# Performance work log

Hardware: AMD Instinct MI355X
Metric: run time of the kernel (lower is better)

## Reference

```python
import jax, jax.numpy as jnp
import numpy as np

N, E, D_IN, D_H, D_OUT = 100000, 1600000, 128, 128, 47
BN_EPS = 1e-5


def setup_inputs() -> dict:
    key = jax.random.key(0)
    ks = jax.random.split(key, 12)
    x = jax.random.normal(ks[0], (N, D_IN), dtype=jnp.float32)
    edge_index = jax.random.randint(ks[1], (2, E), 0, N, dtype=jnp.int64)
    s = 1.0 / np.sqrt(D_H)
    return {
        "x": x,
        "edge_index": edge_index,
        "W1": jax.random.normal(ks[2], (D_IN, D_H), dtype=jnp.float32) * s,
        "b1": jnp.zeros((D_H,), dtype=jnp.float32),
        "gamma": jax.random.uniform(ks[3], (D_H,), dtype=jnp.float32, minval=0.5, maxval=1.5),
        "beta": jax.random.normal(ks[4], (D_H,), dtype=jnp.float32) * 0.1,
        "mean": jax.random.normal(ks[5], (D_H,), dtype=jnp.float32) * 0.1,
        "var": jax.random.uniform(ks[6], (D_H,), dtype=jnp.float32, minval=0.5, maxval=1.5),
        "W2": jax.random.normal(ks[7], (D_H, D_H), dtype=jnp.float32) * s,
        "b2": jnp.zeros((D_H,), dtype=jnp.float32),
        "Wf": jax.random.normal(ks[8], (D_H, D_OUT), dtype=jnp.float32) * s,
        "bf": jnp.zeros((D_OUT,), dtype=jnp.float32),
    }


def gcn_conv(x, src, dst, W, b, n):
    # x' = x @ W, then symmetric-normalized aggregation with self-loops (PyG GCNConv).
    h = x @ W
    loops = jnp.arange(n, dtype=src.dtype)
    s = jnp.concatenate([src, loops])
    d = jnp.concatenate([dst, loops])
    deg = jax.ops.segment_sum(jnp.ones_like(d, dtype=h.dtype), d, num_segments=n)
    dinv = jnp.where(deg > 0, jax.lax.rsqrt(deg), 0.0)
    norm = dinv[s] * dinv[d]                      # [E+N]
    msg = h[s] * norm[:, None]                    # [E+N, D] gather
    out = jax.ops.segment_sum(msg, d, num_segments=n)  # scatter-add
    return out + b


def reference(x, edge_index, W1, b1, gamma, beta, mean, var, W2, b2, Wf, bf):
    n = x.shape[0]
    src, dst = edge_index[0], edge_index[1]
    # layer 1: GCNConv -> BatchNorm (eval) -> ReLU -> dropout (identity in eval)
    h1 = gcn_conv(x, src, dst, W1, b1, n)
    h1 = (h1 - mean) * jax.lax.rsqrt(var + BN_EPS) * gamma + beta
    h1 = jax.nn.relu(h1)
    # layer 2 (last conv, no BN/act)
    h2 = gcn_conv(h1, src, dst, W2, b2, n)
    # JumpingKnowledge max over layer outputs
    jk = jnp.maximum(h1, h2)
    logits = jk @ Wf + bf
    return jax.nn.log_softmax(logits, axis=1)
```

## Files before the change

kernel.cpp:

```cpp
#include <hip/hip_runtime.h>
#include <math.h>

#define DH 128
#define DOUT 47
#define BN_EPS 1e-5f

#define NCH 64
#define RS 32768
#define RSH 15

typedef __attribute__((ext_vector_type(8))) short short8;
typedef __attribute__((ext_vector_type(4))) float float4v;
typedef __attribute__((ext_vector_type(2))) float float2v;

__device__ __forceinline__ unsigned bf16_rne(float f) {
    unsigned u = __float_as_uint(f);
    return (u + 0x7fffu + ((u >> 16) & 1u)) >> 16;
}
__device__ __forceinline__ unsigned pack_bf2(float a, float b) {
    return (bf16_rne(a) & 0xffffu) | (bf16_rne(b) << 16);
}
__device__ __forceinline__ float2 unpack_bf2(unsigned u) {
    return make_float2(__uint_as_float(u << 16),
                       __uint_as_float(u & 0xffff0000u));
}


__global__ __launch_bounds__(256) void prep_k(const float* __restrict__ W1,
                                              const float* __restrict__ W2,
                                              unsigned* __restrict__ W1b,
                                              unsigned* __restrict__ W2b,
                                              unsigned* __restrict__ bufA, int n,
                                              int* __restrict__ el, int elsz4) {
    int tid = threadIdx.x;
    if (blockIdx.x >= 2) {
        int i4 = (blockIdx.x - 2) * 256 + tid;
        if (i4 < elsz4) *(int4*)(el + (size_t)i4 * 4) = make_int4(n, n, n, n);
        return;
    }
    const float* W = blockIdx.x ? W2 : W1;
    unsigned* Wb = blockIdx.x ? W2b : W1b;
    if (blockIdx.x == 0 && tid < 64) bufA[(size_t)n * 64 + tid] = 0;
    for (int p = tid; p < 128 * 32; p += 256) {
        int nn = p >> 5;
        int k0 = (p & 31) << 2;
        float f0 = W[(size_t)(k0 + 0) * 128 + nn];
        float f1 = W[(size_t)(k0 + 1) * 128 + nn];
        float f2 = W[(size_t)(k0 + 2) * 128 + nn];
        float f3 = W[(size_t)(k0 + 3) * 128 + nn];
        uint2 v;
        v.x = pack_bf2(f0, f1);
        v.y = pack_bf2(f2, f3);
        *(uint2*)(Wb + (size_t)nn * 64 + (k0 >> 1)) = v;
    }
}

__global__ __launch_bounds__(256) void hist_rank_k(const int* __restrict__ dst,
                                                   int* __restrict__ rank,
                                                   int* __restrict__ cntM,
                                                   int e, int ce, int nr,
                                                   size_t nsp) {
    __shared__ int bins[RS];
    int tid = threadIdx.x;
    int r = blockIdx.x % nr;
    int ch = blockIdx.x / nr;
    {
        int4* b4 = (int4*)bins;
        for (int j = tid; j < RS / 4; j += 256) b4[j] = make_int4(0, 0, 0, 0);
    }
    __syncthreads();
    int lo = ch * ce;
    int hi = lo + ce;
    if (hi > e) hi = e;
    if (lo < hi) {
        int n4end = lo + ((hi - lo) & ~3);
        for (int i0 = lo + tid * 4; i0 < n4end; i0 += 1024) {
            int4 d4 = *(const int4*)(dst + i0);
            if ((d4.x >> RSH) == r) rank[i0 + 0] = atomicAdd(&bins[d4.x & (RS - 1)], 1);
            if ((d4.y >> RSH) == r) rank[i0 + 1] = atomicAdd(&bins[d4.y & (RS - 1)], 1);
            if ((d4.z >> RSH) == r) rank[i0 + 2] = atomicAdd(&bins[d4.z & (RS - 1)], 1);
            if ((d4.w >> RSH) == r) rank[i0 + 3] = atomicAdd(&bins[d4.w & (RS - 1)], 1);
        }
        for (int i0 = n4end + tid; i0 < hi; i0 += 256) {
            int d = dst[i0];
            if ((d >> RSH) == r) rank[i0] = atomicAdd(&bins[d & (RS - 1)], 1);
        }
    }
    __syncthreads();
    {
        int* outp = cntM + (size_t)ch * nsp + ((size_t)r << RSH);
        const int4* b4 = (const int4*)bins;
        int4* o4 = (int4*)outp;
        for (int j = tid; j < RS / 4; j += 256) o4[j] = b4[j];
    }
}

__global__ __launch_bounds__(256) void scan1_k(const int* __restrict__ cntM,
                                               int* __restrict__ counts,
                                               int* __restrict__ offsets,
                                               int* __restrict__ blocksums,
                                               size_t nsp, int n) {
    __shared__ int sd[256];
    int tid = threadIdx.x;
    int base = blockIdx.x * 1024 + tid * 4;
    int v[4];
#pragma unroll
    for (int j = 0; j < 4; j++) {
        int idx = base + j;
        int c = 0;
        if (idx < n) {
            for (int ch = 0; ch < NCH; ch++) c += cntM[(size_t)ch * nsp + idx];
            counts[idx] = c;
            c = (c + 7) & ~7;
        }
        v[j] = c;
    }
    int tsum = v[0] + v[1] + v[2] + v[3];
    sd[tid] = tsum;
    __syncthreads();
    for (int off = 1; off < 256; off <<= 1) {
        int x = (tid >= off) ? sd[tid - off] : 0;
        __syncthreads();
        sd[tid] += x;
        __syncthreads();
    }
    if (tid == 255) blocksums[blockIdx.x] = sd[255];
    int run = sd[tid] - tsum;
    if (base + 0 < n) offsets[base + 0] = run;  run += v[0];
    if (base + 1 < n) offsets[base + 1] = run;  run += v[1];
    if (base + 2 < n) offsets[base + 2] = run;  run += v[2];
    if (base + 3 < n) offsets[base + 3] = run;
}

__global__ __launch_bounds__(128) void scan2_k(int* __restrict__ blocksums, int nb) {
    __shared__ int sd[128];
    int tid = threadIdx.x;
    int v = (tid < nb) ? blocksums[tid] : 0;
    sd[tid] = v;
    __syncthreads();
    for (int off = 1; off < 128; off <<= 1) {
        int x = (tid >= off) ? sd[tid - off] : 0;
        __syncthreads();
        sd[tid] += x;
        __syncthreads();
    }
    if (tid < nb) blocksums[tid] = sd[tid] - v;
}

__global__ void finalize_k(int* __restrict__ offsets,
                           float* __restrict__ dinv,
                           const int* __restrict__ counts,
                           const int* __restrict__ blocksums,
                           int* __restrict__ cntM, size_t nsp, int n) {
    int i = blockIdx.x * 256 + threadIdx.x;
    if (i >= n) return;
    int o = offsets[i] + blocksums[i >> 10];
    offsets[i] = o;
    int run = o;
    for (int ch = 0; ch < NCH; ch++) {
        size_t idx = (size_t)ch * nsp + i;
        int c = cntM[idx];
        cntM[idx] = run;
        run += c;
    }
    int c = counts[i];
    dinv[i] = rsqrtf((float)(c + 1));
}

__global__ __launch_bounds__(256) void fused_sg_k(
    const float* __restrict__ A, const unsigned* __restrict__ Wb,
    unsigned* __restrict__ Cb, int M,
    const int* __restrict__ src, const int* __restrict__ dst,
    const int* __restrict__ rank, const int* __restrict__ baseM,
    const float* __restrict__ dinv, int* __restrict__ el,
    int e, int ce, size_t nsp, int gemmBlocks) {
    __shared__ ushort Bl[128 * 72];
    int bid = blockIdx.x;
    int q = bid >> 1;
    int tid = threadIdx.x;

    if (bid & 1) {
        int i0 = (q * 256 + tid) * 4;
        if (i0 + 4 <= e) {
            int4 s4 = *(const int4*)(src + i0);
            int4 d4 = *(const int4*)(dst + i0);
            int4 r4 = *(const int4*)(rank + i0);
            const int* bM = baseM + (size_t)(i0 / ce) * nsp;
            unsigned qx = (unsigned)(dinv[s4.x] * 32767.f + 0.5f);
            unsigned qy = (unsigned)(dinv[s4.y] * 32767.f + 0.5f);
            unsigned qz = (unsigned)(dinv[s4.z] * 32767.f + 0.5f);
            unsigned qw = (unsigned)(dinv[s4.w] * 32767.f + 0.5f);
            el[bM[d4.x] + r4.x] = (int)((unsigned)s4.x | (qx << 17));
            el[bM[d4.y] + r4.y] = (int)((unsigned)s4.y | (qy << 17));
            el[bM[d4.z] + r4.z] = (int)((unsigned)s4.z | (qz << 17));
            el[bM[d4.w] + r4.w] = (int)((unsigned)s4.w | (qw << 17));
        } else {
            for (int i = i0; i < e; i++) {
                unsigned qv = (unsigned)(dinv[src[i]] * 32767.f + 0.5f);
                int idx = baseM[(size_t)(i / ce) * nsp + dst[i]] + rank[i];
                el[idx] = (int)((unsigned)src[i] | (qv << 17));
            }
        }
        return;
    }

    if (q >= gemmBlocks) return;
    int lane = tid & 63;
    int wv = tid >> 6;
    int quad = lane >> 4;
    int l15 = lane & 15;
    int r0 = q * 64 + wv * 16;
    int mload = r0 + l15;
    if (mload > M - 1) mload = M - 1;
    const float* Ar = A + (size_t)mload * 128 + quad * 8;

    float4v acc[8];
#pragma unroll
    for (int t = 0; t < 8; t++) acc[t] = (float4v){0.f, 0.f, 0.f, 0.f};

    unsigned* Bu = (unsigned*)Bl;
#pragma unroll
    for (int ph = 0; ph < 2; ++ph) {
        if (ph) __syncthreads();
        for (int p = tid; p < 1024; p += 256) {
            int row = p >> 3;
            int c4 = (p & 7) << 2;
            uint4 v = *(const uint4*)(Wb + (size_t)row * 64 + ph * 32 + c4);
            *(uint4*)(Bu + (size_t)row * 36 + c4) = v;
        }
        __syncthreads();
#pragma unroll
        for (int kpl = 0; kpl < 2; ++kpl) {
            int kp = ph * 2 + kpl;
            float4 a0 = *(const float4*)(Ar + kp * 32);
            float4 a1 = *(const float4*)(Ar + kp * 32 + 4);
            float af[8] = {a0.x, a0.y, a0.z, a0.w, a1.x, a1.y, a1.z, a1.w};
            short8 av;
#pragma unroll
            for (int j = 0; j < 8; j++) av[j] = (short)bf16_rne(af[j]);
            int kb = kpl * 32 + quad * 8;
#pragma unroll
            for (int nt = 0; nt < 8; nt++) {
                short8 b8 = *(const short8*)(&Bl[(size_t)(nt * 16 + l15) * 72 + kb]);
                acc[nt] = __builtin_amdgcn_mfma_f32_16x16x32_bf16(av, b8, acc[nt], 0, 0, 0);
            }
        }
    }

    ushort* Cu = (ushort*)Cb;
#pragma unroll
    for (int r = 0; r < 4; r++) {
        int row = r0 + quad * 4 + r;
        if (row < M) {
#pragma unroll
            for (int nt = 0; nt < 8; nt++) {
                Cu[(size_t)row * 128 + nt * 16 + l15] =
                    (ushort)bf16_rne(acc[nt][r]);
            }
        }
    }
}

__global__ __launch_bounds__(256) void gemm_bf16_k(const unsigned* __restrict__ Ab,
                                                   const unsigned* __restrict__ Wb,
                                                   unsigned* __restrict__ Cb, int M) {
    __shared__ ushort Bl[128 * 136];
    int tid = threadIdx.x;
    {
        unsigned* Bu = (unsigned*)Bl;
        for (int q = tid; q < 128 * 16; q += 256) {
            int row = q >> 4;
            int c = (q & 15) << 2;
            uint4 v = *(const uint4*)(Wb + (size_t)row * 64 + c);
            *(uint4*)(Bu + (size_t)row * 68 + c) = v;
        }
    }
    __syncthreads();

    int lane = tid & 63;
    int wv = tid >> 6;
    int quad = lane >> 4;
    int l15 = lane & 15;
    int r0 = blockIdx.x * 64 + wv * 16;
    int mload = r0 + l15;
    if (mload > M - 1) mload = M - 1;
    const unsigned* Ar = Ab + (size_t)mload * 64 + quad * 4;

    float4v acc[8];
#pragma unroll
    for (int t = 0; t < 8; t++) acc[t] = (float4v){0.f, 0.f, 0.f, 0.f};

    for (int kp = 0; kp < 4; ++kp) {
        uint4 a4 = *(const uint4*)(Ar + kp * 16);
        short8 av;
        av[0] = (short)(a4.x & 0xffff); av[1] = (short)(a4.x >> 16);
        av[2] = (short)(a4.y & 0xffff); av[3] = (short)(a4.y >> 16);
        av[4] = (short)(a4.z & 0xffff); av[5] = (short)(a4.z >> 16);
        av[6] = (short)(a4.w & 0xffff); av[7] = (short)(a4.w >> 16);
        int kb = kp * 32 + quad * 8;
#pragma unroll
        for (int nt = 0; nt < 8; nt++) {
            short8 b8 = *(const short8*)(&Bl[(size_t)(nt * 16 + l15) * 136 + kb]);
            acc[nt] = __builtin_amdgcn_mfma_f32_16x16x32_bf16(av, b8, acc[nt], 0, 0, 0);
        }
    }

    ushort* Cu = (ushort*)Cb;
#pragma unroll
    for (int r = 0; r < 4; r++) {
        int row = r0 + quad * 4 + r;
        if (row < M) {
#pragma unroll
            for (int nt = 0; nt < 8; nt++) {
                Cu[(size_t)row * 128 + nt * 16 + l15] =
                    (ushort)bf16_rne(acc[nt][r]);
            }
        }
    }
}

__device__ __forceinline__ float4 agg_core(const uint2* __restrict__ Hu2,
                                           const int* __restrict__ el,
                                           int start, int cnt, int node,
                                           float dvn, int li, int half) {
    float2v a01 = {0.f, 0.f};
    float2v a23 = {0.f, 0.f};
    int groups = ((cnt + 7) & ~7) >> 3;
    if (groups > 0) {
        const int* p = el + start + half * 4;

#define EDGE(cu, rr) {                                                       \
        float qf = (float)((unsigned)(rr) >> 17) * (1.f / 32767.f);          \
        float2v f0, f1;                                                      \
        f0.x = __uint_as_float((cu).x << 16);                                \
        f0.y = __uint_as_float((cu).x & 0xffff0000u);                        \
        f1.x = __uint_as_float((cu).y << 16);                                \
        f1.y = __uint_as_float((cu).y & 0xffff0000u);                        \
        a01.x = fmaf(f0.x, qf, a01.x); a01.y = fmaf(f0.y, qf, a01.y);        \
        a23.x = fmaf(f1.x, qf, a23.x); a23.y = fmaf(f1.y, qf, a23.y);        \
}
        int4 rc = *(const int4*)p;
        uint2 c0 = Hu2[(size_t)(rc.x & 0x1FFFF) * 32 + li];
        uint2 c1 = Hu2[(size_t)(rc.y & 0x1FFFF) * 32 + li];
        uint2 c2 = Hu2[(size_t)(rc.z & 0x1FFFF) * 32 + li];
        uint2 c3 = Hu2[(size_t)(rc.w & 0x1FFFF) * 32 + li];
        int4 rn = *(const int4*)(p + 8);
        for (int g = 0; g < groups; ++g) {
            uint2 n0 = Hu2[(size_t)(rn.x & 0x1FFFF) * 32 + li];
            uint2 n1 = Hu2[(size_t)(rn.y & 0x1FFFF) * 32 + li];
            uint2 n2 = Hu2[(size_t)(rn.z & 0x1FFFF) * 32 + li];
            uint2 n3 = Hu2[(size_t)(rn.w & 0x1FFFF) * 32 + li];
            int4 r2 = *(const int4*)(p + 8 * (g + 2));
            EDGE(c0, rc.x) EDGE(c1, rc.y) EDGE(c2, rc.z) EDGE(c3, rc.w)
            c0 = n0; c1 = n1; c2 = n2; c3 = n3;
            rc = rn; rn = r2;
        }
#undef EDGE
    }
    float4 acc = make_float4(a01.x, a01.y, a23.x, a23.y);
    acc.x += __shfl_xor(acc.x, 32);
    acc.y += __shfl_xor(acc.y, 32);
    acc.z += __shfl_xor(acc.z, 32);
    acc.w += __shfl_xor(acc.w, 32);
    uint2 sv = Hu2[(size_t)node * 32 + li];
    float2 s0 = unpack_bf2(sv.x);
    float2 s1 = unpack_bf2(sv.y);
    acc.x = fmaf(s0.x, dvn, acc.x); acc.y = fmaf(s0.y, dvn, acc.y);
    acc.z = fmaf(s1.x, dvn, acc.z); acc.w = fmaf(s1.y, dvn, acc.w);
    return acc;
}

__global__ __launch_bounds__(256) void agg1_k(
    const unsigned* __restrict__ H, const int* __restrict__ el,
    const int* __restrict__ offsets, const int* __restrict__ counts,
    const float* __restrict__ dinv, const float* __restrict__ b1,
    const float* __restrict__ gamma, const float* __restrict__ beta,
    const float* __restrict__ mean, const float* __restrict__ var,
    unsigned* __restrict__ H1b, int n) {
    int lane = threadIdx.x & 63;
    int li = lane & 31;
    int half = lane >> 5;
    int node = blockIdx.x * 4 + (threadIdx.x >> 6);
    if (node >= n) return;
    float dv = dinv[node];
    float4 acc = agg_core((const uint2*)H, el, offsets[node],
                          counts[node], node, dv, li, half);
    if (half == 0) {
        int f0 = li * 4;
        float4 bb = *(const float4*)(b1 + f0);
        float4 mm = *(const float4*)(mean + f0);
        float4 vv = *(const float4*)(var + f0);
        float4 gg = *(const float4*)(gamma + f0);
        float4 be = *(const float4*)(beta + f0);
        float4 o;
        o.x = fmaxf((acc.x * dv + bb.x - mm.x) * rsqrtf(vv.x + BN_EPS) * gg.x + be.x, 0.f);
        o.y = fmaxf((acc.y * dv + bb.y - mm.y) * rsqrtf(vv.y + BN_EPS) * gg.y + be.y, 0.f);
        o.z = fmaxf((acc.z * dv + bb.z - mm.z) * rsqrtf(vv.z + BN_EPS) * gg.z + be.z, 0.f);
        o.w = fmaxf((acc.w * dv + bb.w - mm.w) * rsqrtf(vv.w + BN_EPS) * gg.w + be.w, 0.f);
        uint2 pk;
        pk.x = pack_bf2(o.x, o.y);
        pk.y = pack_bf2(o.z, o.w);
        *(uint2*)(H1b + (size_t)node * 64 + li * 2) = pk;
    }
}

__global__ __launch_bounds__(256) void agg2_k(
    const unsigned* __restrict__ H, const int* __restrict__ el,
    const int* __restrict__ offsets, const int* __restrict__ counts,
    const float* __restrict__ dinv, const float* __restrict__ b2,
    unsigned* __restrict__ H1b, int n) {
    int lane = threadIdx.x & 63;
    int li = lane & 31;
    int half = lane >> 5;
    int node = blockIdx.x * 4 + (threadIdx.x >> 6);
    if (node >= n) return;
    float dv = dinv[node];
    float4 acc = agg_core((const uint2*)H, el, offsets[node],
                          counts[node], node, dv, li, half);
    if (half == 0) {
        int f0 = li * 4;
        float4 bb = *(const float4*)(b2 + f0);
        uint2* p = (uint2*)(H1b + (size_t)node * 64 + li * 2);
        uint2 hv = *p;
        float2 ha = unpack_bf2(hv.x);
        float2 hb = unpack_bf2(hv.y);
        float4 o;
        o.x = fmaxf(ha.x, acc.x * dv + bb.x);
        o.y = fmaxf(ha.y, acc.y * dv + bb.y);
        o.z = fmaxf(hb.x, acc.z * dv + bb.z);
        o.w = fmaxf(hb.y, acc.w * dv + bb.w);
        uint2 pk;
        pk.x = pack_bf2(o.x, o.y);
        pk.y = pack_bf2(o.z, o.w);
        *p = pk;
    }
}

__global__ __launch_bounds__(256) void head_k(const unsigned* __restrict__ JKb,
                                              const float* __restrict__ Wf,
                                              const float* __restrict__ bf,
                                              float* __restrict__ out, int n) {
    __shared__ __align__(16) float Bs[48 * 132];
    __shared__ __align__(16) float As[64 * 36];
    int tid = threadIdx.x;
    for (int p = tid; p < 47 * 32; p += 256) {
        int c = p >> 5;
        int k0 = (p & 31) << 2;
        float4 v;
        v.x = Wf[(size_t)(k0 + 0) * DOUT + c];
        v.y = Wf[(size_t)(k0 + 1) * DOUT + c];
        v.z = Wf[(size_t)(k0 + 2) * DOUT + c];
        v.w = Wf[(size_t)(k0 + 3) * DOUT + c];
        *(float4*)(&Bs[c * 132 + k0]) = v;
    }
    int tx = tid & 15;
    int ty = tid >> 4;
    int node0 = blockIdx.x * 64;

    float acc[4][3];
#pragma unroll
    for (int i = 0; i < 4; i++)
#pragma unroll
        for (int j = 0; j < 3; j++) acc[i][j] = 0.f;

    for (int kk = 0; kk < 128; kk += 32) {
        __syncthreads();
        for (int l = tid; l < 512; l += 256) {
            int r = l >> 3;
            int c4 = (l & 7) << 2;
            int row = node0 + r;
            float4 v = make_float4(0.f, 0.f, 0.f, 0.f);
            if (row < n) {
                uint2 u = *(const uint2*)(JKb + (size_t)row * 64 + ((kk + c4) >> 1));
                float2 f0 = unpack_bf2(u.x);
                float2 f1 = unpack_bf2(u.y);
                v = make_float4(f0.x, f0.y, f1.x, f1.y);
            }
            *(float4*)(&As[r * 36 + c4]) = v;
        }
        __syncthreads();
#pragma unroll
        for (int k4 = 0; k4 < 32; k4 += 4) {
            float4 a0 = *(const float4*)(&As[(ty * 4 + 0) * 36 + k4]);
            float4 a1 = *(const float4*)(&As[(ty * 4 + 1) * 36 + k4]);
            float4 a2 = *(const float4*)(&As[(ty * 4 + 2) * 36 + k4]);
            float4 a3 = *(const float4*)(&As[(ty * 4 + 3) * 36 + k4]);
            float4 b0 = *(const float4*)(&Bs[(tx * 3 + 0) * 132 + kk + k4]);
            float4 b1 = *(const float4*)(&Bs[(tx * 3 + 1) * 132 + kk + k4]);
            float4 b2 = *(const float4*)(&Bs[(tx * 3 + 2) * 132 + kk + k4]);
#define DOT_ROW(i, a)                                                        \
            acc[i][0] = fmaf(a.x, b0.x, acc[i][0]);                          \
            acc[i][0] = fmaf(a.y, b0.y, acc[i][0]);                          \
            acc[i][0] = fmaf(a.z, b0.z, acc[i][0]);                          \
            acc[i][0] = fmaf(a.w, b0.w, acc[i][0]);                          \
            acc[i][1] = fmaf(a.x, b1.x, acc[i][1]);                          \
            acc[i][1] = fmaf(a.y, b1.y, acc[i][1]);                          \
            acc[i][1] = fmaf(a.z, b1.z, acc[i][1]);                          \
            acc[i][1] = fmaf(a.w, b1.w, acc[i][1]);                          \
            acc[i][2] = fmaf(a.x, b2.x, acc[i][2]);                          \
            acc[i][2] = fmaf(a.y, b2.y, acc[i][2]);                          \
            acc[i][2] = fmaf(a.z, b2.z, acc[i][2]);                          \
            acc[i][2] = fmaf(a.w, b2.w, acc[i][2]);
            DOT_ROW(0, a0)
            DOT_ROW(1, a1)
            DOT_ROW(2, a2)
            DOT_ROW(3, a3)
#undef DOT_ROW
        }
    }

    float bfv[3];
#pragma unroll
    for (int j = 0; j < 3; j++) {
        int c = tx * 3 + j;
        bfv[j] = (c < DOUT) ? bf[c] : 0.f;
    }
#pragma unroll
    for (int i = 0; i < 4; i++) {
        int node = node0 + ty * 4 + i;
        float l0 = acc[i][0] + bfv[0];
        float l1 = acc[i][1] + bfv[1];
        float l2 = acc[i][2] + bfv[2];
        bool v2ok = (tx * 3 + 2) < DOUT;
        float m = fmaxf(l0, l1);
        if (v2ok) m = fmaxf(m, l2);
        for (int off = 8; off >= 1; off >>= 1) m = fmaxf(m, __shfl_xor(m, off));
        float s = expf(l0 - m) + expf(l1 - m) + (v2ok ? expf(l2 - m) : 0.f);
        for (int off = 8; off >= 1; off >>= 1) s += __shfl_xor(s, off);
        float ls = m + logf(s);
        if (node < n) {
            float* o = out + (size_t)node * DOUT + tx * 3;
            o[0] = l0 - ls;
            o[1] = l1 - ls;
            if (v2ok) o[2] = l2 - ls;
        }
    }
}

extern "C" void kernel_launch(void* const* d_in, const int* in_sizes, int n_in,
                              void* d_out, int out_size, void* d_ws, size_t ws_size,
                              hipStream_t stream) {
    const float* x     = (const float*)d_in[0];
    const int*   ei    = (const int*)d_in[1];
    const float* W1    = (const float*)d_in[2];
    const float* b1    = (const float*)d_in[3];
    const float* gamma = (const float*)d_in[4];
    const float* beta  = (const float*)d_in[5];
    const float* mean  = (const float*)d_in[6];
    const float* var   = (const float*)d_in[7];
    const float* W2    = (const float*)d_in[8];
    const float* b2    = (const float*)d_in[9];
    const float* Wf    = (const float*)d_in[10];
    const float* bf    = (const float*)d_in[11];
    float* out = (float*)d_out;

    int N_ = in_sizes[0] / 128;
    int E_ = in_sizes[1] / 2;
    const int* src = ei;
    const int* dst = ei + E_;

    int NR = (N_ + RS - 1) >> RSH;
    size_t NSP = (size_t)NR << RSH;
    int CE = ((E_ + NCH - 1) / NCH + 3) & ~3;
    int elTotal = E_ + 7 * N_ + 128;
    int elsz4 = (elTotal + 3) / 4;

    char* ws = (char*)d_ws;
    unsigned* bufA = (unsigned*)ws; ws += (size_t)(N_ + 1) * 64 * 4;
    size_t h1bSz = (size_t)N_ * 64 * 4;
    size_t cntSz = (size_t)NCH * NSP * 4;
    unsigned* h1b = (unsigned*)ws;
    int* cntM     = (int*)ws;       ws += (h1bSz > cntSz ? h1bSz : cntSz);
    int*   counts  = (int*)ws;    ws += (size_t)N_ * 4;
    int*   offsets = (int*)ws;    ws += (size_t)N_ * 4;
    float* dinv    = (float*)ws;  ws += (size_t)N_ * 4;
    int*   rank    = (int*)ws;    ws += (size_t)E_ * 4;
    int*   el      = (int*)ws;    ws += ((size_t)elsz4 * 4) * 4;
    int*   bsums   = (int*)ws;    ws += 1024 * 4;
    unsigned* W1b  = (unsigned*)ws; ws += 128 * 64 * 4;
    unsigned* W2b  = (unsigned*)ws; ws += 128 * 64 * 4;

    int nb = (N_ + 1023) / 1024;
    int gemmBlocks = (N_ + 63) / 64;
    int scatBlocks = (E_ + 1023) / 1024;
    int pairs = gemmBlocks > scatBlocks ? gemmBlocks : scatBlocks;
    int prepBlocks = 2 + (elsz4 + 255) / 256;

    prep_k<<<prepBlocks, 256, 0, stream>>>(W1, W2, W1b, W2b, bufA, N_, el, elsz4);
    hist_rank_k<<<NCH * NR, 256, 0, stream>>>(dst, rank, cntM, E_, CE, NR, NSP);
    scan1_k<<<nb, 256, 0, stream>>>(cntM, counts, offsets, bsums, NSP, N_);
    scan2_k<<<1, 128, 0, stream>>>(bsums, nb);
    finalize_k<<<(N_ + 255) / 256, 256, 0, stream>>>(offsets, dinv, counts,
                                                     bsums, cntM, NSP, N_);
    fused_sg_k<<<2 * pairs, 256, 0, stream>>>(x, W1b, bufA, N_,
                                              src, dst, rank, cntM, dinv, el,
                                              E_, CE, NSP, gemmBlocks);
    agg1_k<<<(N_ + 3) / 4, 256, 0, stream>>>(bufA, el, offsets, counts, dinv,
                                             b1, gamma, beta, mean, var, h1b, N_);
    gemm_bf16_k<<<gemmBlocks, 256, 0, stream>>>(h1b, W2b, bufA, N_);
    agg2_k<<<(N_ + 3) / 4, 256, 0, stream>>>(bufA, el, offsets, counts, dinv,
                                             b2, h1b, N_);
    head_k<<<(N_ + 63) / 64, 256, 0, stream>>>(h1b, Wf, bf, out, N_);
}
```

Before: 421.8 us.

## Move layer-1 GEMM into scan kernel and scatter edges via LDS-cached bases

The layer-1 GEMM now runs as extra blocks of the first scan kernel instead of being interleaved with the edge scatter. The edge scatter becomes its own kernel, partitioned by chunk and dst range like the histogram. Each block copies its slice of per-chunk base offsets into LDS, so the scattered global reads of baseM become LDS lookups. The cost is that every block rereads its whole edge chunk for each dst range, and the GEMM blocks reserve a large LDS buffer inside the scan kernel, which may reduce occupancy for the scan blocks.

Measured after the change: 422.6 us. About the same (+0.2%).

```diff
diff --git a/kernel.cpp b/kernel.cpp
--- a/kernel.cpp
+++ b/kernel.cpp
@@ -95,41 +95,101 @@
     }
 }
 
-__global__ __launch_bounds__(256) void scan1_k(const int* __restrict__ cntM,
-                                               int* __restrict__ counts,
-                                               int* __restrict__ offsets,
-                                               int* __restrict__ blocksums,
-                                               size_t nsp, int n) {
+__global__ __launch_bounds__(256) void scan1g_k(
+    const int* __restrict__ cntM, int* __restrict__ counts,
+    int* __restrict__ offsets, int* __restrict__ blocksums,
+    size_t nsp, int n, int nb,
+    const float* __restrict__ A, const unsigned* __restrict__ Wb,
+    unsigned* __restrict__ Cb, int M) {
+    __shared__ ushort Bl[128 * 136];
     __shared__ int sd[256];
     int tid = threadIdx.x;
-    int base = blockIdx.x * 1024 + tid * 4;
-    int v[4];
-#pragma unroll
-    for (int j = 0; j < 4; j++) {
-        int idx = base + j;
-        int c = 0;
-        if (idx < n) {
-            for (int ch = 0; ch < NCH; ch++) c += cntM[(size_t)ch * nsp + idx];
-            counts[idx] = c;
-            c = (c + 7) & ~7;
-        }
-        v[j] = c;
-    }
-    int tsum = v[0] + v[1] + v[2] + v[3];
-    sd[tid] = tsum;
+    int bid = blockIdx.x;
+
+    if (bid < nb) {
+        int base = bid * 1024 + tid * 4;
+        int v[4];
+#pragma unroll
+        for (int j = 0; j < 4; j++) {
+            int idx = base + j;
+            int c = 0;
+            if (idx < n) {
+                for (int ch = 0; ch < NCH; ch++) c += cntM[(size_t)ch * nsp + idx];
+                counts[idx] = c;
+                c = (c + 7) & ~7;
+            }
+            v[j] = c;
+        }
+        int tsum = v[0] + v[1] + v[2] + v[3];
+        sd[tid] = tsum;
+        __syncthreads();
+        for (int off = 1; off < 256; off <<= 1) {
+            int x = (tid >= off) ? sd[tid - off] : 0;
+            __syncthreads();
+            sd[tid] += x;
+            __syncthreads();
+        }
+        if (tid == 255) blocksums[bid] = sd[255];
+        int run = sd[tid] - tsum;
+        if (base + 0 < n) offsets[base + 0] = run;  run += v[0];
+        if (base + 1 < n) offsets[base + 1] = run;  run += v[1];
+        if (base + 2 < n) offsets[base + 2] = run;  run += v[2];
+        if (base + 3 < n) offsets[base + 3] = run;
+        return;
+    }
+
+    int q = bid - nb;
+    {
+        unsigned* Bu = (unsigned*)Bl;
+        for (int p = tid; p < 128 * 16; p += 256) {
+            int row = p >> 4;
+            int c = (p & 15) << 2;
+            uint4 v = *(const uint4*)(Wb + (size_t)row * 64 + c);
+            *(uint4*)(Bu + (size_t)row * 68 + c) = v;
+        }
+    }
     __syncthreads();
-    for (int off = 1; off < 256; off <<= 1) {
-        int x = (tid >= off) ? sd[tid - off] : 0;
-        __syncthreads();
-        sd[tid] += x;
-        __syncthreads();
-    }
-    if (tid == 255) blocksums[blockIdx.x] = sd[255];
-    int run = sd[tid] - tsum;
-    if (base + 0 < n) offsets[base + 0] = run;  run += v[0];
-    if (base + 1 < n) offsets[base + 1] = run;  run += v[1];
-    if (base + 2 < n) offsets[base + 2] = run;  run += v[2];
-    if (base + 3 < n) offsets[base + 3] = run;
+
+    int lane = tid & 63;
+    int wv = tid >> 6;
+    int quad = lane >> 4;
+    int l15 = lane & 15;
+    int r0 = q * 64 + wv * 16;
+    int mload = r0 + l15;
+    if (mload > M - 1) mload = M - 1;
+    const float* Ar = A + (size_t)mload * 128 + quad * 8;
+
+    float4v acc[8];
+#pragma unroll
+    for (int t = 0; t < 8; t++) acc[t] = (float4v){0.f, 0.f, 0.f, 0.f};
+
+    for (int kp = 0; kp < 4; ++kp) {
+        float4 a0 = *(const float4*)(Ar + kp * 32);
+        float4 a1 = *(const float4*)(Ar + kp * 32 + 4);
+        float af[8] = {a0.x, a0.y, a0.z, a0.w, a1.x, a1.y, a1.z, a1.w};
+        short8 av;
+#pragma unroll
+        for (int j = 0; j < 8; j++) av[j] = (short)bf16_rne(af[j]);
+        int kb = kp * 32 + quad * 8;
+#pragma unroll
+        for (int nt = 0; nt < 8; nt++) {
+            short8 b8 = *(const short8*)(&Bl[(size_t)(nt * 16 + l15) * 136 + kb]);
+            acc[nt] = __builtin_amdgcn_mfma_f32_16x16x32_bf16(av, b8, acc[nt], 0, 0, 0);
+        }
+    }
+
+    ushort* Cu = (ushort*)Cb;
+#pragma unroll
+    for (int r = 0; r < 4; r++) {
+        int row = r0 + quad * 4 + r;
+        if (row < M) {
+#pragma unroll
+            for (int nt = 0; nt < 8; nt++) {
+                Cu[(size_t)row * 128 + nt * 16 + l15] =
+                    (ushort)bf16_rne(acc[nt][r]);
+            }
+        }
+    }
 }
 
 __global__ __launch_bounds__(128) void scan2_k(int* __restrict__ blocksums, int nb) {
@@ -167,96 +227,53 @@
     dinv[i] = rsqrtf((float)(c + 1));
 }
 
-__global__ __launch_bounds__(256) void fused_sg_k(
-    const float* __restrict__ A, const unsigned* __restrict__ Wb,
-    unsigned* __restrict__ Cb, int M,
+__global__ __launch_bounds__(256) void scatter_lds_k(
     const int* __restrict__ src, const int* __restrict__ dst,
     const int* __restrict__ rank, const int* __restrict__ baseM,
     const float* __restrict__ dinv, int* __restrict__ el,
-    int e, int ce, size_t nsp, int gemmBlocks) {
-    __shared__ ushort Bl[128 * 72];
-    int bid = blockIdx.x;
-    int q = bid >> 1;
+    int e, int ce, int nr, size_t nsp) {
+    __shared__ int bins[RS];
     int tid = threadIdx.x;
-
-    if (bid & 1) {
-        int i0 = (q * 256 + tid) * 4;
-        if (i0 + 4 <= e) {
-            int4 s4 = *(const int4*)(src + i0);
-            int4 d4 = *(const int4*)(dst + i0);
-            int4 r4 = *(const int4*)(rank + i0);
-            const int* bM = baseM + (size_t)(i0 / ce) * nsp;
-            unsigned qx = (unsigned)(dinv[s4.x] * 32767.f + 0.5f);
-            unsigned qy = (unsigned)(dinv[s4.y] * 32767.f + 0.5f);
-            unsigned qz = (unsigned)(dinv[s4.z] * 32767.f + 0.5f);
-            unsigned qw = (unsigned)(dinv[s4.w] * 32767.f + 0.5f);
-            el[bM[d4.x] + r4.x] = (int)((unsigned)s4.x | (qx << 17));
-            el[bM[d4.y] + r4.y] = (int)((unsigned)s4.y | (qy << 17));
-            el[bM[d4.z] + r4.z] = (int)((unsigned)s4.z | (qz << 17));
-            el[bM[d4.w] + r4.w] = (int)((unsigned)s4.w | (qw << 17));
-        } else {
-            for (int i = i0; i < e; i++) {
-                unsigned qv = (unsigned)(dinv[src[i]] * 32767.f + 0.5f);
-                int idx = baseM[(size_t)(i / ce) * nsp + dst[i]] + rank[i];
-                el[idx] = (int)((unsigned)src[i] | (qv << 17));
-            }
-        }
-        return;
-    }
-
-    if (q >= gemmBlocks) return;
-    int lane = tid & 63;
-    int wv = tid >> 6;
-    int quad = lane >> 4;
-    int l15 = lane & 15;
-    int r0 = q * 64 + wv * 16;
-    int mload = r0 + l15;
-    if (mload > M - 1) mload = M - 1;
-    const float* Ar = A + (size_t)mload * 128 + quad * 8;
-
-    float4v acc[8];
-#pragma unroll
-    for (int t = 0; t < 8; t++) acc[t] = (float4v){0.f, 0.f, 0.f, 0.f};
-
-    unsigned* Bu = (unsigned*)Bl;
-#pragma unroll
-    for (int ph = 0; ph < 2; ++ph) {
-        if (ph) __syncthreads();
-        for (int p = tid; p < 1024; p += 256) {
-            int row = p >> 3;
-            int c4 = (p & 7) << 2;
-            uint4 v = *(const uint4*)(Wb + (size_t)row * 64 + ph * 32 + c4);
-            *(uint4*)(Bu + (size_t)row * 36 + c4) = v;
-        }
-        __syncthreads();
-#pragma unroll
-        for (int kpl = 0; kpl < 2; ++kpl) {
-            int kp = ph * 2 + kpl;
-            float4 a0 = *(const float4*)(Ar + kp * 32);
-            float4 a1 = *(const float4*)(Ar + kp * 32 + 4);
-            float af[8] = {a0.x, a0.y, a0.z, a0.w, a1.x, a1.y, a1.z, a1.w};
-            short8 av;
-#pragma unroll
-            for (int j = 0; j < 8; j++) av[j] = (short)bf16_rne(af[j]);
-            int kb = kpl * 32 + quad * 8;
-#pragma unroll
-            for (int nt = 0; nt < 8; nt++) {
-                short8 b8 = *(const short8*)(&Bl[(size_t)(nt * 16 + l15) * 72 + kb]);
-                acc[nt] = __builtin_amdgcn_mfma_f32_16x16x32_bf16(av, b8, acc[nt], 0, 0, 0);
-            }
-        }
-    }
-
-    ushort* Cu = (ushort*)Cb;
-#pragma unroll
-    for (int r = 0; r < 4; r++) {
-        int row = r0 + quad * 4 + r;
-        if (row < M) {
-#pragma unroll
-            for (int nt = 0; nt < 8; nt++) {
-                Cu[(size_t)row * 128 + nt * 16 + l15] =
-                    (ushort)bf16_rne(acc[nt][r]);
-            }
+    int r = blockIdx.x % nr;
+    int ch = blockIdx.x / nr;
+    {
+        const int4* s4 = (const int4*)(baseM + (size_t)ch * nsp + ((size_t)r << RSH));
+        int4* b4 = (int4*)bins;
+        for (int j = tid; j < RS / 4; j += 256) b4[j] = s4[j];
+    }
+    __syncthreads();
+    int lo = ch * ce;
+    int hi = lo + ce;
+    if (hi > e) hi = e;
+    if (lo >= hi) return;
+    int n4end = lo + ((hi - lo) & ~3);
+    for (int i0 = lo + tid * 4; i0 < n4end; i0 += 1024) {
+        int4 d4 = *(const int4*)(dst + i0);
+        int4 s4 = *(const int4*)(src + i0);
+        int4 r4 = *(const int4*)(rank + i0);
+        if ((d4.x >> RSH) == r) {
+            unsigned q = (unsigned)(dinv[s4.x] * 32767.f + 0.5f);
+            el[bins[d4.x & (RS - 1)] + r4.x] = (int)((unsigned)s4.x | (q << 17));
+        }
+        if ((d4.y >> RSH) == r) {
+            unsigned q = (unsigned)(dinv[s4.y] * 32767.f + 0.5f);
+            el[bins[d4.y & (RS - 1)] + r4.y] = (int)((unsigned)s4.y | (q << 17));
+        }
+        if ((d4.z >> RSH) == r) {
+            unsigned q = (unsigned)(dinv[s4.z] * 32767.f + 0.5f);
+            el[bins[d4.z & (RS - 1)] + r4.z] = (int)((unsigned)s4.z | (q << 17));
+        }
+        if ((d4.w >> RSH) == r) {
+            unsigned q = (unsigned)(dinv[s4.w] * 32767.f + 0.5f);
+            el[bins[d4.w & (RS - 1)] + r4.w] = (int)((unsigned)s4.w | (q << 17));
+        }
+    }
+    for (int i = n4end + tid; i < hi; i += 256) {
+        int d = dst[i];
+        if ((d >> RSH) == r) {
+            int s = src[i];
+            unsigned q = (unsigned)(dinv[s] * 32767.f + 0.5f);
+            el[bins[d & (RS - 1)] + rank[i]] = (int)((unsigned)s | (q << 17));
         }
     }
 }
@@ -582,19 +599,18 @@
 
     int nb = (N_ + 1023) / 1024;
     int gemmBlocks = (N_ + 63) / 64;
-    int scatBlocks = (E_ + 1023) / 1024;
-    int pairs = gemmBlocks > scatBlocks ? gemmBlocks : scatBlocks;
     int prepBlocks = 2 + (elsz4 + 255) / 256;
 
     prep_k<<<prepBlocks, 256, 0, stream>>>(W1, W2, W1b, W2b, bufA, N_, el, elsz4);
     hist_rank_k<<<NCH * NR, 256, 0, stream>>>(dst, rank, cntM, E_, CE, NR, NSP);
-    scan1_k<<<nb, 256, 0, stream>>>(cntM, counts, offsets, bsums, NSP, N_);
+    scan1g_k<<<nb + gemmBlocks, 256, 0, stream>>>(cntM, counts, offsets, bsums,
+                                                  NSP, N_, nb,
+                                                  x, W1b, bufA, N_);
     scan2_k<<<1, 128, 0, stream>>>(bsums, nb);
     finalize_k<<<(N_ + 255) / 256, 256, 0, stream>>>(offsets, dinv, counts,
                                                      bsums, cntM, NSP, N_);
-    fused_sg_k<<<2 * pairs, 256, 0, stream>>>(x, W1b, bufA, N_,
-                                              src, dst, rank, cntM, dinv, el,
-                                              E_, CE, NSP, gemmBlocks);
+    scatter_lds_k<<<NCH * NR, 256, 0, stream>>>(src, dst, rank, cntM, dinv, el,
+                                                E_, CE, NR, NSP);
     agg1_k<<<(N_ + 3) / 4, 256, 0, stream>>>(bufA, el, offsets, counts, dinv,
                                              b1, gamma, beta, mean, var, h1b, N_);
     gemm_bf16_k<<<gemmBlocks, 256, 0, stream>>>(h1b, W2b, bufA, N_);
```
